# Kernel tuning notes

Hardware: AMD Instinct MI355X
Metric: run time of the kernel (lower is better)

The kernel has to match this reference:

```python
import jax, jax.numpy as jnp
import numpy as np

N_NODES = 100000
N_EDGES = 1600000
IN_CH = 64
HID = 64
N_LAYERS = 4


def setup_inputs() -> dict:
    key = jax.random.key(0)
    ks = jax.random.split(key, 12)
    x = jax.random.normal(ks[0], (N_NODES, IN_CH), dtype=jnp.float32)
    edge_index = jax.random.randint(ks[1], (2, N_EDGES), 0, N_NODES, dtype=jnp.int64)
    s = 1.0 / np.sqrt(HID)
    W_enc = jax.random.normal(ks[2], (IN_CH, HID), dtype=jnp.float32) * s
    b_enc = jnp.zeros((HID,), dtype=jnp.float32)
    Wg = jax.random.normal(ks[3], (N_LAYERS, HID, HID), dtype=jnp.float32) * s
    bg = jnp.zeros((N_LAYERS, HID), dtype=jnp.float32)
    # MLPReadout: 64 -> 32 -> 16 -> 1
    W0 = jax.random.normal(ks[4], (HID, HID // 2), dtype=jnp.float32) * s
    b0 = jnp.zeros((HID // 2,), dtype=jnp.float32)
    W1 = jax.random.normal(ks[5], (HID // 2, HID // 4), dtype=jnp.float32) * (1.0 / np.sqrt(HID // 2))
    b1 = jnp.zeros((HID // 4,), dtype=jnp.float32)
    W2 = jax.random.normal(ks[6], (HID // 4, 1), dtype=jnp.float32) * (1.0 / np.sqrt(HID // 4))
    b2 = jnp.zeros((1,), dtype=jnp.float32)
    return {"x": x, "edge_index": edge_index, "W_enc": W_enc, "b_enc": b_enc,
            "Wg": Wg, "bg": bg, "W0": W0, "b0": b0, "W1": W1, "b1": b1,
            "W2": W2, "b2": b2}


def _gcn_norm(edge_index, n_nodes):
    # PyG GCNConv default: add self-loops, symmetric normalization.
    loop = jnp.arange(n_nodes, dtype=edge_index.dtype)
    src = jnp.concatenate([edge_index[0], loop])  # [E + N]
    dst = jnp.concatenate([edge_index[1], loop])
    deg = jax.ops.segment_sum(jnp.ones_like(dst, dtype=jnp.float32), dst,
                              num_segments=n_nodes)
    dinv = jnp.where(deg > 0, 1.0 / jnp.sqrt(deg), 0.0)
    norm = dinv[src] * dinv[dst]  # [E + N]
    return src, dst, norm


def reference(x, edge_index, W_enc, b_enc, Wg, bg, W0, b0, W1, b1, W2, b2):
    n_nodes = x.shape[0]
    src, dst, norm = _gcn_norm(edge_index, n_nodes)
    h = x @ W_enc + b_enc  # feature encoder [N, HID]
    n_layers = Wg.shape[0]
    for l in range(n_layers):
        h_res = h
        hw = h @ Wg[l]                                  # [N, HID] GEMM
        msg = hw[src] * norm[:, None]                   # gather + scale
        h = jax.ops.segment_sum(msg, dst, num_segments=n_nodes) + bg[l]
        h = h + h_res                                   # residual
        if l != n_layers - 1:
            # dropout in eval mode is identity
            h = jax.nn.relu(h)
    # MLPReadout (L=2)
    y = jax.nn.relu(h @ W0 + b0)
    y = jax.nn.relu(y @ W1 + b1)
    y = y @ W2 + b2  # [N, 1]
    return y
```

## Files before the change

kernel.cpp:

```cpp
#include <hip/hip_runtime.h>

typedef __attribute__((ext_vector_type(8))) short bf16x8_t;
typedef __attribute__((ext_vector_type(4))) float f32x4_t;


__global__ void k_zero(int* __restrict__ p, int n) {
    int i = threadIdx.x;
    if (i < n) p[i] = 0;
}


#define PCHUNK 4096
#define PTHREADS 512
#define EPT (PCHUNK / PTHREADS)
#define NBUCK_MAX 400
#define BCAP 6144

__global__ __launch_bounds__(PTHREADS)
void k_partition2(const int* __restrict__ src, const int* __restrict__ dst,
                  int* __restrict__ bcnt, unsigned int* __restrict__ stageg,
                  int E, int nbuck) {
    __shared__ int hist[NBUCK_MAX];
    __shared__ int boffs[NBUCK_MAX];
    __shared__ int cur[NBUCK_MAX];
    __shared__ int gbase[NBUCK_MAX];
    __shared__ int tmp[PTHREADS];
    __shared__ unsigned int stage[PCHUNK];
    __shared__ unsigned short sbid[PCHUNK];

    int tid = threadIdx.x;
    int ebase = blockIdx.x * PCHUNK;
    int ecount = min(PCHUNK, E - ebase);

    if (tid < NBUCK_MAX) hist[tid] = 0;
    __syncthreads();

    int dreg[EPT], sreg[EPT];
#pragma unroll
    for (int k = 0; k < EPT; k++) {
        int e = ebase + tid + k * PTHREADS;
        if (tid + k * PTHREADS < ecount) {
            dreg[k] = dst[e];
            sreg[k] = src[e];
            atomicAdd(&hist[dreg[k] >> 8], 1);
        } else dreg[k] = -1;
    }
    __syncthreads();

    int v = (tid < nbuck) ? hist[tid] : 0;
    tmp[tid] = v;
    __syncthreads();
    for (int d = 1; d < PTHREADS; d <<= 1) {
        int t = (tid >= d) ? tmp[tid - d] : 0;
        __syncthreads();
        tmp[tid] += t;
        __syncthreads();
    }
    if (tid < nbuck) { boffs[tid] = tmp[tid] - v; cur[tid] = tmp[tid] - v; }
    __syncthreads();

#pragma unroll
    for (int k = 0; k < EPT; k++) {
        if (dreg[k] >= 0) {
            int b = dreg[k] >> 8;
            int p = atomicAdd(&cur[b], 1);
            stage[p] = ((unsigned int)(dreg[k] & 255) << 17) | (unsigned int)sreg[k];
            sbid[p] = (unsigned short)b;
        }
    }
    __syncthreads();

    if (tid < nbuck) {
        int c = cur[tid] - boffs[tid];
        if (c > 0) gbase[tid] = atomicAdd(&bcnt[tid], c);
    }
    __syncthreads();

    for (int i = tid; i < ecount; i += PTHREADS) {
        int b = sbid[i];
        stageg[(size_t)b * BCAP + gbase[b] + (i - boffs[b])] = stage[i];
    }
}


__global__ __launch_bounds__(512)
void k_bucket_scan(const int* __restrict__ bcnt, int* __restrict__ bbase, int nbuck) {
    __shared__ int tmp[512];
    int tid = threadIdx.x;
    int v = (tid < nbuck) ? bcnt[tid] : 0;
    tmp[tid] = v;
    __syncthreads();
    for (int d = 1; d < 512; d <<= 1) {
        int t = (tid >= d) ? tmp[tid - d] : 0;
        __syncthreads();
        tmp[tid] += t;
        __syncthreads();
    }
    if (tid < nbuck) bbase[tid] = tmp[tid] - v;
    if (tid == nbuck - 1) bbase[nbuck] = tmp[tid];
}


__global__ __launch_bounds__(1024)
void k_finefill2(const unsigned int* __restrict__ stageg, const int* __restrict__ bcnt,
                 const int* __restrict__ bbase, int* __restrict__ offs,
                 float* __restrict__ dinv, int* __restrict__ col, int N, int nbuck) {
    __shared__ int cnt0[256];
    __shared__ int excl[256];
    __shared__ int cur[256];
    __shared__ unsigned int stage[BCAP];
    int b = blockIdx.x;
    int tid = threadIdx.x;
    int nbase = b << 8;
    int nn = min(256, N - nbase);
    int n = bcnt[b];
    int base = bbase[b];
    const unsigned int* sg = stageg + (size_t)b * BCAP;

    if (tid < 256) cnt0[tid] = 0;
    __syncthreads();

    for (int i = tid; i < n; i += 1024)
        atomicAdd(&cnt0[sg[i] >> 17], 1);
    __syncthreads();

    if (tid < 256) excl[tid] = cnt0[tid];
    __syncthreads();
    for (int d = 1; d < 256; d <<= 1) {
        int t = 0;
        if (tid < 256 && tid >= d) t = excl[tid - d];
        __syncthreads();
        if (tid < 256) excl[tid] += t;
        __syncthreads();
    }
    if (tid < 256) {
        int e = excl[tid] - cnt0[tid];
        cur[tid] = e;
        if (tid < nn) {
            offs[nbase + tid] = base + e;
            dinv[nbase + tid] = rsqrtf((float)(cnt0[tid] + 1));
        }
    }
    if (b == nbuck - 1 && tid == 0) offs[N] = bbase[nbuck];
    __syncthreads();

    for (int i = tid; i < n; i += 1024) {
        unsigned int v = sg[i];
        int p = atomicAdd(&cur[v >> 17], 1);
        stage[p] = v & 0x1FFFFu;
    }
    __syncthreads();
    for (int i = tid; i < n; i += 1024)
        col[base + i] = (int)stage[i];
}


__device__ __forceinline__ unsigned int bf16rne(float x) {
    unsigned int u = __float_as_uint(x);
    return (u + 0x7FFFu + ((u >> 16) & 1u)) >> 16;
}
__device__ __forceinline__ float u2flo(unsigned int u) { return __uint_as_float(u << 16); }
__device__ __forceinline__ float u2fhi(unsigned int u) { return __uint_as_float(u & 0xFFFF0000u); }

__device__ __forceinline__ void split2(float a, float b, unsigned int& hi, unsigned int& lo) {
    unsigned int ha = bf16rne(a), hb = bf16rne(b);
    float ra = a - u2flo(ha), rb = b - u2flo(hb);
    hi = ha | (hb << 16);
    lo = bf16rne(ra) | (bf16rne(rb) << 16);
}

union FragU { uint4 u4; bf16x8_t bf; };


__global__ __launch_bounds__(256)
void k_wsplit(const float* __restrict__ Wenc, const float* __restrict__ Wg,
              unsigned int* __restrict__ wfragg) {
    int m = blockIdx.x;
    const float* W = (m == 0) ? Wenc : (Wg + (size_t)(m - 1) * 4096);
    unsigned int* wb = wfragg + (size_t)m * 4096;
    int tid = threadIdx.x;
#pragma unroll
    for (int i = 0; i < 16; i++) {
        int flat = tid * 16 + i;
        int mm = flat & 3;
        int l = (flat >> 2) & 63;
        int fp = flat >> 8;
        int p = fp & 1;
        int f = fp >> 1;
        int ct = f >> 1, kh = f & 1;
        int k = kh * 32 + ((l >> 4) << 3) + 2 * mm;
        int c = ct * 16 + (l & 15);
        float w0 = W[k * 64 + c];
        float w1 = W[(k + 1) * 64 + c];
        unsigned int hi, lo;
        split2(w0, w1, hi, lo);
        wb[flat] = p ? lo : hi;
    }
}


template <bool HAS_BIAS, bool SCALE, bool OUTBF16>
__global__ __launch_bounds__(256, 4)
void k_gemm_mfma(const float* __restrict__ A, const uint4* __restrict__ wfrag,
                 const float* __restrict__ bias, const float* __restrict__ scale,
                 void* __restrict__ out, int N) {
    int tid = threadIdx.x;
    int lane = tid & 63;
    int wv = tid >> 6;
    int rowbase = blockIdx.x * 64 + wv * 16;

    FragU ahi[2], alo[2];
    {
        int row = rowbase + (lane & 15);
        int rc = min(row, N - 1);
        float dv = SCALE ? scale[rc] : 1.0f;
#pragma unroll
        for (int kh = 0; kh < 2; kh++) {
            const float4* hp = (const float4*)(A + (size_t)rc * 64 + kh * 32 + ((lane >> 4) << 3));
            float4 p0 = hp[0], p1 = hp[1];
            p0.x *= dv; p0.y *= dv; p0.z *= dv; p0.w *= dv;
            p1.x *= dv; p1.y *= dv; p1.z *= dv; p1.w *= dv;
            split2(p0.x, p0.y, ahi[kh].u4.x, alo[kh].u4.x);
            split2(p0.z, p0.w, ahi[kh].u4.y, alo[kh].u4.y);
            split2(p1.x, p1.y, ahi[kh].u4.z, alo[kh].u4.z);
            split2(p1.z, p1.w, ahi[kh].u4.w, alo[kh].u4.w);
        }
    }

    f32x4_t acc[4];
#pragma unroll
    for (int ct = 0; ct < 4; ct++) {
        float b = HAS_BIAS ? bias[ct * 16 + (lane & 15)] : 0.0f;
        acc[ct] = (f32x4_t){b, b, b, b};
    }

#pragma unroll
    for (int ct = 0; ct < 4; ct++) {
#pragma unroll
        for (int kh = 0; kh < 2; kh++) {
            FragU bhi, blo;
            bhi.u4 = wfrag[((ct * 2 + kh) * 2 + 0) * 64 + lane];
            blo.u4 = wfrag[((ct * 2 + kh) * 2 + 1) * 64 + lane];
            acc[ct] = __builtin_amdgcn_mfma_f32_16x16x32_bf16(ahi[kh].bf, bhi.bf, acc[ct], 0, 0, 0);
            acc[ct] = __builtin_amdgcn_mfma_f32_16x16x32_bf16(alo[kh].bf, bhi.bf, acc[ct], 0, 0, 0);
            acc[ct] = __builtin_amdgcn_mfma_f32_16x16x32_bf16(ahi[kh].bf, blo.bf, acc[ct], 0, 0, 0);
        }
    }

    if (OUTBF16) {
        unsigned short* ob = (unsigned short*)out;
#pragma unroll
        for (int ct = 0; ct < 4; ct++) {
#pragma unroll
            for (int r = 0; r < 4; r++) {
                float v = acc[ct][r];
                float vo = __shfl_xor(v, 1);
                int row = rowbase + ((lane >> 4) << 2) + r;
                if (!(lane & 1) && row < N) {
                    unsigned int pk = bf16rne(v) | (bf16rne(vo) << 16);
                    *(unsigned int*)(ob + (size_t)row * 64 + ct * 16 + (lane & 15)) = pk;
                }
            }
        }
    } else {
        float* of = (float*)out;
#pragma unroll
        for (int ct = 0; ct < 4; ct++) {
#pragma unroll
            for (int r = 0; r < 4; r++) {
                int row = rowbase + ((lane >> 4) << 2) + r;
                if (row < N)
                    of[(size_t)row * 64 + ct * 16 + (lane & 15)] = acc[ct][r];
            }
        }
    }
}


__global__ __launch_bounds__(256, 4)
void k_agg_fused(const unsigned short* __restrict__ hwb_in, const int* __restrict__ offs,
                 const int* __restrict__ col, const float* __restrict__ dinv,
                 const float* __restrict__ bg, float* __restrict__ h,
                 const uint4* __restrict__ wnext, unsigned short* __restrict__ hwb_out,
                 int N) {
    int tid = threadIdx.x;
    int t = blockIdx.x * 256 + tid;
    int wid = t >> 6;
    int lane = tid & 63;
    int G = lane >> 3;
    int L = lane & 7;
    int node = wid * 8 + G;
    bool valid = node < N;
    int nc = valid ? node : N - 1;

    int start = offs[nc];
    int end = valid ? offs[nc + 1] : start;

    uint4 v = ((const uint4*)(hwb_in + (size_t)nc * 64))[L];
    float a0 = u2flo(v.x), a1 = u2fhi(v.x);
    float a2 = u2flo(v.y), a3 = u2fhi(v.y);
    float a4 = u2flo(v.z), a5 = u2fhi(v.z);
    float a6 = u2flo(v.w), a7 = u2fhi(v.w);

    for (int e = start;; e += 2) {
        bool act0 = e < end;
        if (__ballot(act0) == 0ULL) break;
        bool act1 = e + 1 < end;
        int e0 = act0 ? e : 0;
        int e1 = act1 ? e + 1 : 0;
        int s0 = col[e0];
        int s1 = col[e1];
        uint4 v0 = ((const uint4*)(hwb_in + (size_t)s0 * 64))[L];
        uint4 v1 = ((const uint4*)(hwb_in + (size_t)s1 * 64))[L];
        if (!act0) { v0.x = 0u; v0.y = 0u; v0.z = 0u; v0.w = 0u; }
        if (!act1) { v1.x = 0u; v1.y = 0u; v1.z = 0u; v1.w = 0u; }
        a0 += u2flo(v0.x) + u2flo(v1.x);
        a1 += u2fhi(v0.x) + u2fhi(v1.x);
        a2 += u2flo(v0.y) + u2flo(v1.y);
        a3 += u2fhi(v0.y) + u2fhi(v1.y);
        a4 += u2flo(v0.z) + u2flo(v1.z);
        a5 += u2fhi(v0.z) + u2fhi(v1.z);
        a6 += u2flo(v0.w) + u2flo(v1.w);
        a7 += u2fhi(v0.w) + u2fhi(v1.w);
    }

    float dn = dinv[nc];
    float* hrow = h + (size_t)nc * 64 + L * 8;
    float4 r0 = ((const float4*)hrow)[0];
    float4 r1 = ((const float4*)hrow)[1];
    const float* bgp = bg + L * 8;
    float4 b0 = ((const float4*)bgp)[0];
    float4 b1 = ((const float4*)bgp)[1];
    float4 o0, o1;
    o0.x = fmaxf(fmaf(dn, a0, b0.x + r0.x), 0.f);
    o0.y = fmaxf(fmaf(dn, a1, b0.y + r0.y), 0.f);
    o0.z = fmaxf(fmaf(dn, a2, b0.z + r0.z), 0.f);
    o0.w = fmaxf(fmaf(dn, a3, b0.w + r0.w), 0.f);
    o1.x = fmaxf(fmaf(dn, a4, b1.x + r1.x), 0.f);
    o1.y = fmaxf(fmaf(dn, a5, b1.y + r1.y), 0.f);
    o1.z = fmaxf(fmaf(dn, a6, b1.z + r1.z), 0.f);
    o1.w = fmaxf(fmaf(dn, a7, b1.w + r1.w), 0.f);
    if (valid) {
        ((float4*)hrow)[0] = o0;
        ((float4*)hrow)[1] = o1;
    }

    float sv0 = o0.x * dn, sv1 = o0.y * dn, sv2 = o0.z * dn, sv3 = o0.w * dn;
    float sv4 = o1.x * dn, sv5 = o1.y * dn, sv6 = o1.z * dn, sv7 = o1.w * dn;

    int r = lane & 15;
    int kb = lane >> 4;
    int srcA = (r & 7) * 8 + kb;
    int srcB = (r & 7) * 8 + 4 + kb;

    FragU ahi0, alo0, ahi1, alo1;
    {
        float c0 = __shfl(sv0, srcA), c1 = __shfl(sv1, srcA);
        float c2 = __shfl(sv2, srcA), c3 = __shfl(sv3, srcA);
        float c4 = __shfl(sv4, srcA), c5 = __shfl(sv5, srcA);
        float c6 = __shfl(sv6, srcA), c7 = __shfl(sv7, srcA);
        split2(c0, c1, ahi0.u4.x, alo0.u4.x);
        split2(c2, c3, ahi0.u4.y, alo0.u4.y);
        split2(c4, c5, ahi0.u4.z, alo0.u4.z);
        split2(c6, c7, ahi0.u4.w, alo0.u4.w);
    }
    {
        float c0 = __shfl(sv0, srcB), c1 = __shfl(sv1, srcB);
        float c2 = __shfl(sv2, srcB), c3 = __shfl(sv3, srcB);
        float c4 = __shfl(sv4, srcB), c5 = __shfl(sv5, srcB);
        float c6 = __shfl(sv6, srcB), c7 = __shfl(sv7, srcB);
        split2(c0, c1, ahi1.u4.x, alo1.u4.x);
        split2(c2, c3, ahi1.u4.y, alo1.u4.y);
        split2(c4, c5, ahi1.u4.z, alo1.u4.z);
        split2(c6, c7, ahi1.u4.w, alo1.u4.w);
    }

    f32x4_t acc[4];
#pragma unroll
    for (int ct = 0; ct < 4; ct++) acc[ct] = (f32x4_t){0.f, 0.f, 0.f, 0.f};

#pragma unroll
    for (int ct = 0; ct < 4; ct++) {
        FragU bh0, bl0, bh1, bl1;
        bh0.u4 = wnext[((ct * 2 + 0) * 2 + 0) * 64 + lane];
        bl0.u4 = wnext[((ct * 2 + 0) * 2 + 1) * 64 + lane];
        bh1.u4 = wnext[((ct * 2 + 1) * 2 + 0) * 64 + lane];
        bl1.u4 = wnext[((ct * 2 + 1) * 2 + 1) * 64 + lane];
        acc[ct] = __builtin_amdgcn_mfma_f32_16x16x32_bf16(ahi0.bf, bh0.bf, acc[ct], 0, 0, 0);
        acc[ct] = __builtin_amdgcn_mfma_f32_16x16x32_bf16(alo0.bf, bh0.bf, acc[ct], 0, 0, 0);
        acc[ct] = __builtin_amdgcn_mfma_f32_16x16x32_bf16(ahi0.bf, bl0.bf, acc[ct], 0, 0, 0);
        acc[ct] = __builtin_amdgcn_mfma_f32_16x16x32_bf16(ahi1.bf, bh1.bf, acc[ct], 0, 0, 0);
        acc[ct] = __builtin_amdgcn_mfma_f32_16x16x32_bf16(alo1.bf, bh1.bf, acc[ct], 0, 0, 0);
        acc[ct] = __builtin_amdgcn_mfma_f32_16x16x32_bf16(ahi1.bf, bl1.bf, acc[ct], 0, 0, 0);
    }

    int wbase = wid * 8;
#pragma unroll
    for (int ct = 0; ct < 4; ct++) {
#pragma unroll
        for (int rr = 0; rr < 4; rr++) {
            float vv = acc[ct][rr];
            float vo = __shfl_xor(vv, 1);
            int orow = ((lane >> 4) << 2) + rr;
            int onode = wbase + orow;
            if (!(lane & 1) && orow < 8 && onode < N) {
                unsigned int pk = bf16rne(vv) | (bf16rne(vo) << 16);
                *(unsigned int*)(hwb_out + (size_t)onode * 64 + ct * 16 + (lane & 15)) = pk;
            }
        }
    }
}


__global__ __launch_bounds__(256)
void k_agg(const unsigned short* __restrict__ hwb, const int* __restrict__ offs,
           const int* __restrict__ col, const float* __restrict__ dinv,
           const float* __restrict__ bg, float* __restrict__ h, int N, int relu) {
    int t = blockIdx.x * blockDim.x + threadIdx.x;
    int wid = t >> 6;
    int lane = threadIdx.x & 63;
    int G = lane >> 3;
    int L = lane & 7;
    int node = wid * 8 + G;
    bool valid = node < N;
    int nc = valid ? node : N - 1;

    int start = offs[nc];
    int end = valid ? offs[nc + 1] : start;

    uint4 v = ((const uint4*)(hwb + (size_t)nc * 64))[L];
    float a0 = u2flo(v.x), a1 = u2fhi(v.x);
    float a2 = u2flo(v.y), a3 = u2fhi(v.y);
    float a4 = u2flo(v.z), a5 = u2fhi(v.z);
    float a6 = u2flo(v.w), a7 = u2fhi(v.w);

    for (int e = start;; e += 2) {
        bool act0 = e < end;
        if (__ballot(act0) == 0ULL) break;
        bool act1 = e + 1 < end;
        int e0 = act0 ? e : 0;
        int e1 = act1 ? e + 1 : 0;
        int s0 = col[e0];
        int s1 = col[e1];
        uint4 v0 = ((const uint4*)(hwb + (size_t)s0 * 64))[L];
        uint4 v1 = ((const uint4*)(hwb + (size_t)s1 * 64))[L];
        if (!act0) { v0.x = 0u; v0.y = 0u; v0.z = 0u; v0.w = 0u; }
        if (!act1) { v1.x = 0u; v1.y = 0u; v1.z = 0u; v1.w = 0u; }
        a0 += u2flo(v0.x) + u2flo(v1.x);
        a1 += u2fhi(v0.x) + u2fhi(v1.x);
        a2 += u2flo(v0.y) + u2flo(v1.y);
        a3 += u2fhi(v0.y) + u2fhi(v1.y);
        a4 += u2flo(v0.z) + u2flo(v1.z);
        a5 += u2fhi(v0.z) + u2fhi(v1.z);
        a6 += u2flo(v0.w) + u2flo(v1.w);
        a7 += u2fhi(v0.w) + u2fhi(v1.w);
    }

    if (valid) {
        float dn = dinv[node];
        float* hrow = h + (size_t)node * 64 + L * 8;
        float4 r0 = ((const float4*)hrow)[0];
        float4 r1 = ((const float4*)hrow)[1];
        const float* bgp = bg + L * 8;
        float4 b0 = ((const float4*)bgp)[0];
        float4 b1 = ((const float4*)bgp)[1];
        float4 o0, o1;
        o0.x = fmaf(dn, a0, b0.x + r0.x);
        o0.y = fmaf(dn, a1, b0.y + r0.y);
        o0.z = fmaf(dn, a2, b0.z + r0.z);
        o0.w = fmaf(dn, a3, b0.w + r0.w);
        o1.x = fmaf(dn, a4, b1.x + r1.x);
        o1.y = fmaf(dn, a5, b1.y + r1.y);
        o1.z = fmaf(dn, a6, b1.z + r1.z);
        o1.w = fmaf(dn, a7, b1.w + r1.w);
        if (relu) {
            o0.x = fmaxf(o0.x, 0.f); o0.y = fmaxf(o0.y, 0.f);
            o0.z = fmaxf(o0.z, 0.f); o0.w = fmaxf(o0.w, 0.f);
            o1.x = fmaxf(o1.x, 0.f); o1.y = fmaxf(o1.y, 0.f);
            o1.z = fmaxf(o1.z, 0.f); o1.w = fmaxf(o1.w, 0.f);
        }
        ((float4*)hrow)[0] = o0;
        ((float4*)hrow)[1] = o1;
    }
}


__global__ __launch_bounds__(256)
void k_readout(const float* __restrict__ h,
               const float* __restrict__ W0, const float* __restrict__ b0,
               const float* __restrict__ W1, const float* __restrict__ b1,
               const float* __restrict__ W2, const float* __restrict__ b2,
               float* __restrict__ out, int N) {
    int r = blockIdx.x * 256 + threadIdx.x;
    if (r >= N) return;

    float t0[32];
#pragma unroll
    for (int c = 0; c < 32; c++) t0[c] = b0[c];

    const float4* h4 = (const float4*)(h + (size_t)r * 64);
#pragma unroll
    for (int k4 = 0; k4 < 16; k4++) {
        float4 v = h4[k4];
#pragma unroll
        for (int kk = 0; kk < 4; kk++) {
            float xk = (kk == 0) ? v.x : (kk == 1) ? v.y : (kk == 2) ? v.z : v.w;
            const float* wr = W0 + (k4 * 4 + kk) * 32;
#pragma unroll
            for (int c = 0; c < 32; c++) t0[c] = fmaf(xk, wr[c], t0[c]);
        }
    }
#pragma unroll
    for (int c = 0; c < 32; c++) t0[c] = fmaxf(t0[c], 0.f);

    float t1[16];
#pragma unroll
    for (int c = 0; c < 16; c++) t1[c] = b1[c];
#pragma unroll
    for (int k = 0; k < 32; k++) {
        const float* wr = W1 + k * 16;
#pragma unroll
        for (int c = 0; c < 16; c++) t1[c] = fmaf(t0[k], wr[c], t1[c]);
    }
#pragma unroll
    for (int c = 0; c < 16; c++) t1[c] = fmaxf(t1[c], 0.f);

    float y = b2[0];
#pragma unroll
    for (int k = 0; k < 16; k++) y = fmaf(t1[k], W2[k], y);
    out[r] = y;
}


extern "C" void kernel_launch(void* const* d_in, const int* in_sizes, int n_in,
                              void* d_out, int out_size, void* d_ws, size_t ws_size,
                              hipStream_t stream) {
    const float* x     = (const float*)d_in[0];
    const int*   eidx  = (const int*)d_in[1];
    const float* W_enc = (const float*)d_in[2];
    const float* b_enc = (const float*)d_in[3];
    const float* Wg    = (const float*)d_in[4];
    const float* bg    = (const float*)d_in[5];
    const float* W0    = (const float*)d_in[6];
    const float* b0    = (const float*)d_in[7];
    const float* W1    = (const float*)d_in[8];
    const float* b1    = (const float*)d_in[9];
    const float* W2    = (const float*)d_in[10];
    const float* b2    = (const float*)d_in[11];

    int N = in_sizes[0] / 64;
    int E = in_sizes[1] / 2;
    const int* esrc = eidx;
    const int* edst = eidx + E;
    int nbuck = (N + 255) >> 8;

    char* w = (char*)d_ws;
    auto alloc = [&](size_t bytes) -> char* {
        char* p = w;
        w += (bytes + 255) & ~(size_t)255;
        return p;
    };
    int*   bcnt  = (int*)alloc(512 * 4);
    int*   bbase = (int*)alloc(512 * 4);
    int*   offs  = (int*)alloc((size_t)(N + 1) * 4);
    int*   col   = (int*)alloc((size_t)E * 4);
    unsigned int* stageg = (unsigned int*)alloc((size_t)nbuck * BCAP * 4);
    float* dinv  = (float*)alloc((size_t)N * 4);
    float* h     = (float*)alloc((size_t)N * 64 * 4);
    unsigned short* hwbA = (unsigned short*)alloc((size_t)N * 64 * 2);
    unsigned short* hwbB = (unsigned short*)alloc((size_t)N * 64 * 2);
    unsigned int* wfragg = (unsigned int*)alloc(5 * 4096 * 4);

    k_zero<<<1, 512, 0, stream>>>(bcnt, 512);
    k_wsplit<<<5, 256, 0, stream>>>(W_enc, Wg, wfragg);
    k_partition2<<<(E + PCHUNK - 1) / PCHUNK, PTHREADS, 0, stream>>>(esrc, edst, bcnt, stageg, E, nbuck);
    k_bucket_scan<<<1, 512, 0, stream>>>(bcnt, bbase, nbuck);
    k_finefill2<<<nbuck, 1024, 0, stream>>>(stageg, bcnt, bbase, offs, dinv, col, N, nbuck);

    int gbM = (N + 63) / 64;
    int gb = (N + 255) / 256;
    int aggthreads = ((N + 7) / 8) * 64;
    int aggblocks = (aggthreads + 255) / 256;

    k_gemm_mfma<true, false, false><<<gbM, 256, 0, stream>>>(
        x, (const uint4*)wfragg, b_enc, nullptr, h, N);
    k_gemm_mfma<false, true, true><<<gbM, 256, 0, stream>>>(
        h, (const uint4*)(wfragg + (size_t)1 * 4096), nullptr, dinv, hwbA, N);
    k_agg_fused<<<aggblocks, 256, 0, stream>>>(hwbA, offs, col, dinv, bg + 0 * 64, h,
                                               (const uint4*)(wfragg + (size_t)2 * 4096), hwbB, N);
    k_agg_fused<<<aggblocks, 256, 0, stream>>>(hwbB, offs, col, dinv, bg + 1 * 64, h,
                                               (const uint4*)(wfragg + (size_t)3 * 4096), hwbA, N);
    k_agg_fused<<<aggblocks, 256, 0, stream>>>(hwbA, offs, col, dinv, bg + 2 * 64, h,
                                               (const uint4*)(wfragg + (size_t)4 * 4096), hwbB, N);
    k_agg<<<aggblocks, 256, 0, stream>>>(hwbB, offs, col, dinv, bg + 3 * 64, h, N, 0);
    k_readout<<<gb, 256, 0, stream>>>(h, W0, b0, W1, b1, W2, b2, (float*)d_out, N);
}
```

Before: 264.3 us.

## Fuse encoder GEMM with first layer GEMM and stage weights in LDS

The encoder GEMM and the first GCN layer GEMM are merged into one kernel. The encoder output is written to h and also staged, scaled by dinv, in shared memory, where it is re-split into bf16 hi/lo fragments for the second MFMA product. This avoids one launch and a full N×64 fp32 round trip through global memory. Separately, the fused aggregation kernel now copies the next layer's weight fragments into LDS once per block instead of each wave reading them from global memory, at the cost of 16 KB of LDS and an extra barrier per block.

Result: faster. 256.5 us (-3.0%).

```diff
diff --git a/kernel.cpp b/kernel.cpp
--- a/kernel.cpp
+++ b/kernel.cpp
@@ -199,27 +199,26 @@
 }
 
 
-template <bool HAS_BIAS, bool SCALE, bool OUTBF16>
-__global__ __launch_bounds__(256, 4)
-void k_gemm_mfma(const float* __restrict__ A, const uint4* __restrict__ wfrag,
-                 const float* __restrict__ bias, const float* __restrict__ scale,
-                 void* __restrict__ out, int N) {
+__global__ __launch_bounds__(256)
+void k_enc_fused(const float* __restrict__ x, const uint4* __restrict__ wfE,
+                 const float* __restrict__ benc, const uint4* __restrict__ wfG,
+                 const float* __restrict__ dinv, float* __restrict__ h,
+                 unsigned short* __restrict__ hwb_out, int N) {
+    __shared__ float hlds[64 * 68];
+
     int tid = threadIdx.x;
     int lane = tid & 63;
-    int wv = tid >> 6;
-    int rowbase = blockIdx.x * 64 + wv * 16;
+    int w = tid >> 6;
+    int rowbase = blockIdx.x * 64 + w * 16;
 
     FragU ahi[2], alo[2];
     {
         int row = rowbase + (lane & 15);
         int rc = min(row, N - 1);
-        float dv = SCALE ? scale[rc] : 1.0f;
 #pragma unroll
         for (int kh = 0; kh < 2; kh++) {
-            const float4* hp = (const float4*)(A + (size_t)rc * 64 + kh * 32 + ((lane >> 4) << 3));
+            const float4* hp = (const float4*)(x + (size_t)rc * 64 + kh * 32 + ((lane >> 4) << 3));
             float4 p0 = hp[0], p1 = hp[1];
-            p0.x *= dv; p0.y *= dv; p0.z *= dv; p0.w *= dv;
-            p1.x *= dv; p1.y *= dv; p1.z *= dv; p1.w *= dv;
             split2(p0.x, p0.y, ahi[kh].u4.x, alo[kh].u4.x);
             split2(p0.z, p0.w, ahi[kh].u4.y, alo[kh].u4.y);
             split2(p1.x, p1.y, ahi[kh].u4.z, alo[kh].u4.z);
@@ -230,47 +229,71 @@
     f32x4_t acc[4];
 #pragma unroll
     for (int ct = 0; ct < 4; ct++) {
-        float b = HAS_BIAS ? bias[ct * 16 + (lane & 15)] : 0.0f;
+        float b = benc[ct * 16 + (lane & 15)];
         acc[ct] = (f32x4_t){b, b, b, b};
     }
-
 #pragma unroll
     for (int ct = 0; ct < 4; ct++) {
 #pragma unroll
         for (int kh = 0; kh < 2; kh++) {
             FragU bhi, blo;
-            bhi.u4 = wfrag[((ct * 2 + kh) * 2 + 0) * 64 + lane];
-            blo.u4 = wfrag[((ct * 2 + kh) * 2 + 1) * 64 + lane];
+            bhi.u4 = wfE[((ct * 2 + kh) * 2 + 0) * 64 + lane];
+            blo.u4 = wfE[((ct * 2 + kh) * 2 + 1) * 64 + lane];
             acc[ct] = __builtin_amdgcn_mfma_f32_16x16x32_bf16(ahi[kh].bf, bhi.bf, acc[ct], 0, 0, 0);
             acc[ct] = __builtin_amdgcn_mfma_f32_16x16x32_bf16(alo[kh].bf, bhi.bf, acc[ct], 0, 0, 0);
             acc[ct] = __builtin_amdgcn_mfma_f32_16x16x32_bf16(ahi[kh].bf, blo.bf, acc[ct], 0, 0, 0);
         }
     }
 
-    if (OUTBF16) {
-        unsigned short* ob = (unsigned short*)out;
-#pragma unroll
-        for (int ct = 0; ct < 4; ct++) {
-#pragma unroll
-            for (int r = 0; r < 4; r++) {
-                float v = acc[ct][r];
-                float vo = __shfl_xor(v, 1);
-                int row = rowbase + ((lane >> 4) << 2) + r;
-                if (!(lane & 1) && row < N) {
-                    unsigned int pk = bf16rne(v) | (bf16rne(vo) << 16);
-                    *(unsigned int*)(ob + (size_t)row * 64 + ct * 16 + (lane & 15)) = pk;
-                }
-            }
-        }
-    } else {
-        float* of = (float*)out;
-#pragma unroll
-        for (int ct = 0; ct < 4; ct++) {
-#pragma unroll
-            for (int r = 0; r < 4; r++) {
-                int row = rowbase + ((lane >> 4) << 2) + r;
-                if (row < N)
-                    of[(size_t)row * 64 + ct * 16 + (lane & 15)] = acc[ct][r];
+    float dv[4];
+#pragma unroll
+    for (int r = 0; r < 4; r++) {
+        int row = rowbase + ((lane >> 4) << 2) + r;
+        dv[r] = dinv[min(row, N - 1)];
+    }
+#pragma unroll
+    for (int ct = 0; ct < 4; ct++) {
+#pragma unroll
+        for (int r = 0; r < 4; r++) {
+            int row = rowbase + ((lane >> 4) << 2) + r;
+            float v = acc[ct][r];
+            if (row < N) h[(size_t)row * 64 + ct * 16 + (lane & 15)] = v;
+            hlds[(w * 16 + ((lane >> 4) << 2) + r) * 68 + ct * 16 + (lane & 15)] = v * dv[r];
+        }
+    }
+    __syncthreads();
+
+    FragU a2hi[2], a2lo[2];
+#pragma unroll
+    for (int kh = 0; kh < 2; kh++) {
+        const float4* hp = (const float4*)(hlds + (w * 16 + (lane & 15)) * 68 + kh * 32 + ((lane >> 4) << 3));
+        float4 p0 = hp[0], p1 = hp[1];
+        split2(p0.x, p0.y, a2hi[kh].u4.x, a2lo[kh].u4.x);
+        split2(p0.z, p0.w, a2hi[kh].u4.y, a2lo[kh].u4.y);
+        split2(p1.x, p1.y, a2hi[kh].u4.z, a2lo[kh].u4.z);
+        split2(p1.z, p1.w, a2hi[kh].u4.w, a2lo[kh].u4.w);
+    }
+
+#pragma unroll
+    for (int ct = 0; ct < 4; ct++) {
+        f32x4_t a2 = (f32x4_t){0.f, 0.f, 0.f, 0.f};
+#pragma unroll
+        for (int kh = 0; kh < 2; kh++) {
+            FragU bhi, blo;
+            bhi.u4 = wfG[((ct * 2 + kh) * 2 + 0) * 64 + lane];
+            blo.u4 = wfG[((ct * 2 + kh) * 2 + 1) * 64 + lane];
+            a2 = __builtin_amdgcn_mfma_f32_16x16x32_bf16(a2hi[kh].bf, bhi.bf, a2, 0, 0, 0);
+            a2 = __builtin_amdgcn_mfma_f32_16x16x32_bf16(a2lo[kh].bf, bhi.bf, a2, 0, 0, 0);
+            a2 = __builtin_amdgcn_mfma_f32_16x16x32_bf16(a2hi[kh].bf, blo.bf, a2, 0, 0, 0);
+        }
+#pragma unroll
+        for (int r = 0; r < 4; r++) {
+            float v = a2[r];
+            float vo = __shfl_xor(v, 1);
+            int row = rowbase + ((lane >> 4) << 2) + r;
+            if (!(lane & 1) && row < N) {
+                unsigned int pk = bf16rne(v) | (bf16rne(vo) << 16);
+                *(unsigned int*)(hwb_out + (size_t)row * 64 + ct * 16 + (lane & 15)) = pk;
             }
         }
     }
@@ -283,7 +306,14 @@
                  const float* __restrict__ bg, float* __restrict__ h,
                  const uint4* __restrict__ wnext, unsigned short* __restrict__ hwb_out,
                  int N) {
+    __shared__ uint4 wlds[16 * 64];
+
     int tid = threadIdx.x;
+#pragma unroll
+    for (int i = 0; i < 4; i++)
+        wlds[tid + i * 256] = wnext[tid + i * 256];
+    __syncthreads();
+
     int t = blockIdx.x * 256 + tid;
     int wid = t >> 6;
     int lane = tid & 63;
@@ -382,10 +412,10 @@
 #pragma unroll
     for (int ct = 0; ct < 4; ct++) {
         FragU bh0, bl0, bh1, bl1;
-        bh0.u4 = wnext[((ct * 2 + 0) * 2 + 0) * 64 + lane];
-        bl0.u4 = wnext[((ct * 2 + 0) * 2 + 1) * 64 + lane];
-        bh1.u4 = wnext[((ct * 2 + 1) * 2 + 0) * 64 + lane];
-        bl1.u4 = wnext[((ct * 2 + 1) * 2 + 1) * 64 + lane];
+        bh0.u4 = wlds[((ct * 2 + 0) * 2 + 0) * 64 + lane];
+        bl0.u4 = wlds[((ct * 2 + 0) * 2 + 1) * 64 + lane];
+        bh1.u4 = wlds[((ct * 2 + 1) * 2 + 0) * 64 + lane];
+        bl1.u4 = wlds[((ct * 2 + 1) * 2 + 1) * 64 + lane];
         acc[ct] = __builtin_amdgcn_mfma_f32_16x16x32_bf16(ahi0.bf, bh0.bf, acc[ct], 0, 0, 0);
         acc[ct] = __builtin_amdgcn_mfma_f32_16x16x32_bf16(alo0.bf, bh0.bf, acc[ct], 0, 0, 0);
         acc[ct] = __builtin_amdgcn_mfma_f32_16x16x32_bf16(ahi0.bf, bl0.bf, acc[ct], 0, 0, 0);
@@ -577,15 +607,14 @@
     k_bucket_scan<<<1, 512, 0, stream>>>(bcnt, bbase, nbuck);
     k_finefill2<<<nbuck, 1024, 0, stream>>>(stageg, bcnt, bbase, offs, dinv, col, N, nbuck);
 
-    int gbM = (N + 63) / 64;
+    int gbE = (N + 63) / 64;
     int gb = (N + 255) / 256;
     int aggthreads = ((N + 7) / 8) * 64;
     int aggblocks = (aggthreads + 255) / 256;
 
-    k_gemm_mfma<true, false, false><<<gbM, 256, 0, stream>>>(
-        x, (const uint4*)wfragg, b_enc, nullptr, h, N);
-    k_gemm_mfma<false, true, true><<<gbM, 256, 0, stream>>>(
-        h, (const uint4*)(wfragg + (size_t)1 * 4096), nullptr, dinv, hwbA, N);
+    k_enc_fused<<<gbE, 256, 0, stream>>>(
+        x, (const uint4*)wfragg, b_enc, (const uint4*)(wfragg + (size_t)1 * 4096),
+        dinv, h, hwbA, N);
     k_agg_fused<<<aggblocks, 256, 0, stream>>>(hwbA, offs, col, dinv, bg + 0 * 64, h,
                                                (const uint4*)(wfragg + (size_t)2 * 4096), hwbB, N);
     k_agg_fused<<<aggblocks, 256, 0, stream>>>(hwbB, offs, col, dinv, bg + 1 * 64, h,
```
